# Optimization experiments

Hardware: AMD Instinct MI355X
Metric: run time of the kernel (lower is better)

## Reference

```python
import jax, jax.numpy as jnp
import numpy as np

N, IN_DIM, OUT_DIM = 8192, 512, 512
ALPHA = 0.2  # leaky relu negative slope
NEG_BIG = -9e15

def _xavier(key, shape, gain=1.414):
    fan_in, fan_out = shape[0], shape[1]
    bound = gain * np.sqrt(6.0 / (fan_in + fan_out))
    return jax.random.uniform(key, shape, jnp.float32, -bound, bound)

def setup_inputs() -> dict:
    key = jax.random.key(0)
    k1, k2, k3, k4 = jax.random.split(key, 4)
    h = jax.random.normal(k1, (N, IN_DIM), jnp.float32)
    adj = jax.random.randint(k2, (N, N), 0, 2, jnp.int32)
    W = _xavier(k3, (IN_DIM, OUT_DIM))
    a = _xavier(k4, (2 * OUT_DIM, 1))
    return {"h": h, "adj": adj, "W": W, "a": a}

def reference(h, adj, W, a):
    Wh = h @ W                              # [N, out]
    # e_ij = leakyrelu(a1 . Wh_i + a2 . Wh_j) without the O(N^2*2d) concat
    a1 = a[:OUT_DIM, 0]                     # [out]
    a2 = a[OUT_DIM:, 0]                     # [out]
    f1 = Wh @ a1                            # [N]
    f2 = Wh @ a2                            # [N]
    e = jax.nn.leaky_relu(f1[:, None] + f2[None, :], negative_slope=ALPHA)
    e = jnp.where(adj > 0, e, NEG_BIG)
    attention = jax.nn.softmax(e, axis=1)   # dropout is identity in eval mode
    h_prime = attention @ Wh                # [N, out]
    return jax.nn.elu(h_prime)              # concat=True branch
```

## Files before the change

### kernel.cpp

```cpp
#include <hip/hip_runtime.h>
#include <stdint.h>

#define NN   8192
#define DIN  512
#define DOUT 512
#define ALPHA 0.2f

typedef float          floatx4  __attribute__((ext_vector_type(4)));
typedef float          floatx2  __attribute__((ext_vector_type(2)));
typedef short          shortx8  __attribute__((ext_vector_type(8)));
typedef unsigned short ushortx4 __attribute__((ext_vector_type(4)));
typedef int            intx2    __attribute__((ext_vector_type(2)));

__device__ inline unsigned short f2bf(float x) {
    union { float f; unsigned u; } v; v.f = x;
    return (unsigned short)((v.u + 0x7FFFu + ((v.u >> 16) & 1u)) >> 16);
}
__device__ inline unsigned encf(float x) {
    union { float f; unsigned u; } v; v.f = x;
    return (v.u & 0x80000000u) ? ~v.u : (v.u | 0x80000000u);
}
__device__ inline float decf(unsigned e) {
    union { float f; unsigned u; } v;
    v.u = (e & 0x80000000u) ? (e & 0x7FFFFFFFu) : ~e;
    return v.f;
}
__device__ inline float lrelu(float x) { return fmaxf(x, ALPHA * x); }

__global__ __launch_bounds__(256) void transpose_w(const float* __restrict__ W,
                                                   unsigned short* __restrict__ WT) {
    __shared__ float tile[32][33];
    const int t = threadIdx.x;
    const int x = t & 31, y = t >> 5;
    const int tr = (blockIdx.x >> 4) * 32, tc = (blockIdx.x & 15) * 32;
#pragma unroll
    for (int i = 0; i < 4; i++) {
        int r = y + i * 8;
        tile[r][x] = W[(size_t)(tr + r) * DOUT + tc + x];
    }
    __syncthreads();
#pragma unroll
    for (int i = 0; i < 4; i++) {
        int r = y + i * 8;
        WT[(size_t)(tc + r) * DIN + tr + x] = f2bf(tile[x][r]);
    }
}

__global__ __launch_bounds__(256) void gemm_wh(
    const float* __restrict__ h, const unsigned short* __restrict__ WT,
    const float* __restrict__ a, unsigned short* __restrict__ WhTt,
    float* __restrict__ f1, float* __restrict__ f2, unsigned* __restrict__ Menc)
{
    __shared__ float f1s[4][16], f2s[4][16];
    const int t = threadIdx.x;
    const int w = t >> 6, lane = t & 63, l15 = lane & 15, q = lane >> 4;
    const int r0 = blockIdx.x * 16;
    const int wc0 = w * 128;

    floatx4 acc[8];
    const floatx4 z4 = {0.f, 0.f, 0.f, 0.f};
#pragma unroll
    for (int j = 0; j < 8; j++) acc[j] = z4;

    const float* hp = &h[(size_t)(r0 + l15) * DIN + q * 8];
    const unsigned short* bp = &WT[(size_t)(wc0 + l15) * DIN + q * 8];

    floatx4 hA[2][2];
    shortx8 bB[2][8];
    hA[0][0] = *(const floatx4*)hp;
    hA[0][1] = *(const floatx4*)(hp + 4);
#pragma unroll
    for (int nt = 0; nt < 8; nt++)
        bB[0][nt] = *(const shortx8*)(bp + (size_t)nt * 16 * DIN);

#pragma unroll 2
    for (int it = 0; it < 16; ++it) {
        const int c = it & 1, n = c ^ 1;
        const int kn = ((it + 1) & 15) * 32;
        hA[n][0] = *(const floatx4*)(hp + kn);
        hA[n][1] = *(const floatx4*)(hp + kn + 4);
#pragma unroll
        for (int nt = 0; nt < 8; nt++)
            bB[n][nt] = *(const shortx8*)(bp + (size_t)nt * 16 * DIN + kn);

        shortx8 af;
#pragma unroll
        for (int j = 0; j < 8; j++)
            af[j] = (short)f2bf(hA[c][j >> 2][j & 3]);
#pragma unroll
        for (int nt = 0; nt < 8; nt++)
            acc[nt] = __builtin_amdgcn_mfma_f32_16x16x32_bf16(af, bB[c][nt], acc[nt], 0, 0, 0);
    }

    float a1v[8], a2v[8];
#pragma unroll
    for (int nt = 0; nt < 8; nt++) {
        int col = wc0 + nt * 16 + l15;
        a1v[nt] = a[col];
        a2v[nt] = a[DOUT + col];
    }
    {
        const int kk0 = r0 + q * 4;
        const int tile_k = kk0 >> 5;
        const int qq = (kk0 >> 3) & 3;
        const int j0 = kk0 & 7;
#pragma unroll
        for (int nt = 0; nt < 8; nt++) {
            const int tile_n = w * 8 + nt;
            ushortx4 pk;
#pragma unroll
            for (int reg = 0; reg < 4; reg++) pk[reg] = f2bf(acc[nt][reg]);
            *(ushortx4*)&WhTt[(((size_t)tile_k * 32 + tile_n) << 9) + qq * 128 + l15 * 8 + j0] = pk;
        }
    }
    float s1a[4], s2a[4];
#pragma unroll
    for (int reg = 0; reg < 4; reg++) {
        float s1 = 0.f, s2 = 0.f;
#pragma unroll
        for (int nt = 0; nt < 8; nt++) {
            s1 += acc[nt][reg] * a1v[nt];
            s2 += acc[nt][reg] * a2v[nt];
        }
        s1 += __shfl_xor(s1, 1, 64); s2 += __shfl_xor(s2, 1, 64);
        s1 += __shfl_xor(s1, 2, 64); s2 += __shfl_xor(s2, 2, 64);
        s1 += __shfl_xor(s1, 4, 64); s2 += __shfl_xor(s2, 4, 64);
        s1 += __shfl_xor(s1, 8, 64); s2 += __shfl_xor(s2, 8, 64);
        s1a[reg] = s1; s2a[reg] = s2;
    }
    if (l15 == 0) {
#pragma unroll
        for (int reg = 0; reg < 4; reg++) {
            f1s[w][q * 4 + reg] = s1a[reg];
            f2s[w][q * 4 + reg] = s2a[reg];
        }
    }
    __syncthreads();
    if (t < 16) {
        float v1 = f1s[0][t] + f1s[1][t] + f1s[2][t] + f1s[3][t];
        float v2 = f2s[0][t] + f2s[1][t] + f2s[2][t] + f2s[3][t];
        f1[r0 + t] = v1;
        f2[r0 + t] = v2;
        float mx = v2;
        mx = fmaxf(mx, __shfl_xor(mx, 1, 64));
        mx = fmaxf(mx, __shfl_xor(mx, 2, 64));
        mx = fmaxf(mx, __shfl_xor(mx, 4, 64));
        mx = fmaxf(mx, __shfl_xor(mx, 8, 64));
        if (t == 0) atomicMax(Menc, encf(mx));
    }
}

__global__ __launch_bounds__(1024, 4) void gat_agg(
    const int* __restrict__ adj, const unsigned short* __restrict__ WhTt,
    const float* __restrict__ f1, const float* __restrict__ f2,
    const unsigned* __restrict__ Menc, float* __restrict__ out)
{
    __shared__ __align__(16) unsigned short pbuf[2][2][32 * 40];
    __shared__ float red2[32][260];
    __shared__ float lsp[2][16][32];
    __shared__ float linv[32];

    const int t = threadIdx.x;
    const int w = t >> 6, lane = t & 63, l15 = lane & 15, q = lane >> 4;
    const int ks = w >> 3, cw = w & 7;
    const int u = cw * 64 + lane;
    const int prow = u >> 4, pkc = u & 15;
    const int r0 = blockIdx.x * 32;

    const float M = decf(*Menc);
    const float f1v = f1[r0 + prow];
    const float mi = lrelu(f1v + M);

    floatx4 acc[2][4];
    const floatx4 z4 = {0.f, 0.f, 0.f, 0.f};
#pragma unroll
    for (int i = 0; i < 2; i++)
#pragma unroll
        for (int j = 0; j < 4; j++) acc[i][j] = z4;
    float ls = 0.f;

    const unsigned short* bpp = WhTt + (((size_t)(ks * 128) * 32 + cw * 4) << 9) + lane * 8;
    const int* arp = adj + (size_t)(r0 + prow) * NN + ks * 4096 + pkc * 2;
    const float* fpp = f2 + ks * 4096 + pkc * 2;

    intx2    adjr[2];
    floatx2  ffr[2];
    shortx8  breg[2][4];

    adjr[0] = __builtin_nontemporal_load((const intx2*)arp);
    adjr[1] = __builtin_nontemporal_load((const intx2*)(arp + 32));
    ffr[0] = *(const floatx2*)fpp;
    ffr[1] = *(const floatx2*)(fpp + 32);
    {
        float p0 = __expf(lrelu(f1v + ffr[0][0]) - mi);
        float p1 = __expf(lrelu(f1v + ffr[0][1]) - mi);
        p0 = (adjr[0][0] > 0) ? p0 : 0.f;
        p1 = (adjr[0][1] > 0) ? p1 : 0.f;
        ls += p0 + p1;
        unsigned d = __builtin_amdgcn_perm(__float_as_uint(p1), __float_as_uint(p0), 0x07060302u);
        *(unsigned*)&pbuf[ks][0][prow * 40 + pkc * 2] = d;
    }
#pragma unroll
    for (int nt = 0; nt < 4; nt++)
        breg[0][nt] = *(const shortx8*)(bpp + nt * 512);
    __syncthreads();

#pragma unroll 2
    for (int it = 0; it < 128; ++it) {
        const int c = it & 1, n = c ^ 1;
        const int nx = (it + 1) & 127;
        const int nx2 = (it + 2) & 127;

#pragma unroll
        for (int nt = 0; nt < 4; nt++)
            breg[n][nt] = *(const shortx8*)(bpp + (size_t)nx * 16384 + nt * 512);
        const intx2   ad_n = adjr[n];
        const floatx2 ff_n = ffr[n];
        adjr[c] = __builtin_nontemporal_load((const intx2*)(arp + nx2 * 32));
        ffr[c] = *(const floatx2*)(fpp + nx2 * 32);

        if (it < 127) {
            float p0 = __expf(lrelu(f1v + ff_n[0]) - mi);
            float p1 = __expf(lrelu(f1v + ff_n[1]) - mi);
            p0 = (ad_n[0] > 0) ? p0 : 0.f;
            p1 = (ad_n[1] > 0) ? p1 : 0.f;
            ls += p0 + p1;
            unsigned d = __builtin_amdgcn_perm(__float_as_uint(p1), __float_as_uint(p0), 0x07060302u);
            *(unsigned*)&pbuf[ks][n][prow * 40 + pkc * 2] = d;
        }

        const shortx8 af0 = *(const shortx8*)&pbuf[ks][c][l15 * 40 + q * 8];
        const shortx8 af1 = *(const shortx8*)&pbuf[ks][c][(16 + l15) * 40 + q * 8];
#pragma unroll
        for (int nt = 0; nt < 4; nt++) {
            acc[0][nt] = __builtin_amdgcn_mfma_f32_16x16x32_bf16(af0, breg[c][nt], acc[0][nt], 0, 0, 0);
            acc[1][nt] = __builtin_amdgcn_mfma_f32_16x16x32_bf16(af1, breg[c][nt], acc[1][nt], 0, 0, 0);
        }
        __syncthreads();
    }

    lsp[ks][pkc][prow] = ls;
    __syncthreads();
    if (t < 32) {
        float s = 0.f;
#pragma unroll
        for (int g = 0; g < 2; g++)
#pragma unroll
            for (int kc = 0; kc < 16; kc++) s += lsp[g][kc][t];
        linv[t] = 1.f / s;
    }
    __syncthreads();

#pragma unroll 1
    for (int half = 0; half < 2; ++half) {
        const int inHalf = (cw >> 2) == half;
        const int colb = (cw & 3) * 64;
        if (ks == 1 && inHalf) {
#pragma unroll
            for (int mt = 0; mt < 2; mt++)
#pragma unroll
                for (int nt = 0; nt < 4; nt++) {
                    const int col = colb + nt * 16 + l15;
#pragma unroll
                    for (int reg = 0; reg < 4; reg++)
                        red2[mt * 16 + q * 4 + reg][col] = acc[mt][nt][reg];
                }
        }
        __syncthreads();
        if (ks == 0 && inHalf) {
#pragma unroll
            for (int mt = 0; mt < 2; mt++)
#pragma unroll
                for (int nt = 0; nt < 4; nt++) {
                    const int col = colb + nt * 16 + l15;
#pragma unroll
                    for (int reg = 0; reg < 4; reg++) {
                        const int row = mt * 16 + q * 4 + reg;
                        float x = (acc[mt][nt][reg] + red2[row][col]) * linv[row];
                        x = (x > 0.f) ? x : (__expf(x) - 1.f);
                        out[(size_t)(r0 + row) * DOUT + half * 256 + col] = x;
                    }
                }
        }
        __syncthreads();
    }
}

extern "C" void kernel_launch(void* const* d_in, const int* in_sizes, int n_in,
                              void* d_out, int out_size, void* d_ws, size_t ws_size,
                              hipStream_t stream) {
    const float* h   = (const float*)d_in[0];
    const int*   adj = (const int*)d_in[1];
    const float* W   = (const float*)d_in[2];
    const float* a   = (const float*)d_in[3];
    float* out = (float*)d_out;

    char* ws = (char*)d_ws;
    unsigned short* WT    = (unsigned short*)ws;
    unsigned short* WhTt  = (unsigned short*)(ws + 524288);
    float*          f1    = (float*)(ws + 8912896);
    float*          f2    = (float*)(ws + 8945664);
    unsigned*       Menc  = (unsigned*)(ws + 8978432);

    hipMemsetAsync(Menc, 0, 4, stream);
    transpose_w<<<256, 256, 0, stream>>>(W, WT);
    gemm_wh<<<512, 256, 0, stream>>>(h, WT, a, WhTt, f1, f2, Menc);
    gat_agg<<<256, 1024, 0, stream>>>(adj, WhTt, f1, f2, Menc, out);
}
```

Measured before the change: 509.7 us.

## Retile GAT aggregation to 64 rows × 256 cols with XCD-aware block mapping

Each aggregation block now covers 64 output rows and half of the 512 feature columns, where it used to cover 32 rows and all columns. This halves the per-block streaming of the transposed Wh operand and doubles the reuse of each B fragment across four MFMA row tiles. Blocks are remapped so the two column halves of one row group land on the same XCD, hoping adjacency reads hit in the shared L2. In exchange, each adjacency row and its exp/leaky-relu probabilities are read and computed twice, once per column half, and the epilogue is simplified to a single reduction pass.

```diff
diff --git a/kernel.cpp b/kernel.cpp
--- a/kernel.cpp
+++ b/kernel.cpp
@@ -11,6 +11,8 @@
 typedef short          shortx8  __attribute__((ext_vector_type(8)));
 typedef unsigned short ushortx4 __attribute__((ext_vector_type(4)));
 typedef int            intx2    __attribute__((ext_vector_type(2)));
+typedef int            intx4    __attribute__((ext_vector_type(4)));
+typedef unsigned       uintx2   __attribute__((ext_vector_type(2)));
 
 __device__ inline unsigned short f2bf(float x) {
     union { float f; unsigned u; } v; v.f = x;
@@ -155,54 +157,65 @@
     const float* __restrict__ f1, const float* __restrict__ f2,
     const unsigned* __restrict__ Menc, float* __restrict__ out)
 {
-    __shared__ __align__(16) unsigned short pbuf[2][2][32 * 40];
-    __shared__ float red2[32][260];
-    __shared__ float lsp[2][16][32];
-    __shared__ float linv[32];
+    __shared__ __align__(16) unsigned short pbuf[2][2][64 * 40];
+    __shared__ float red2[64][260];
+    __shared__ float lsp[2][8][64];
+    __shared__ float linv[64];
 
     const int t = threadIdx.x;
     const int w = t >> 6, lane = t & 63, l15 = lane & 15, q = lane >> 4;
     const int ks = w >> 3, cw = w & 7;
-    const int u = cw * 64 + lane;
-    const int prow = u >> 4, pkc = u & 15;
-    const int r0 = blockIdx.x * 32;
+    const int u = (w & 7) * 64 + lane;
+    const int prow = u >> 3, pk = u & 7;
+
+    const int xcd = blockIdx.x & 7, sidx = blockIdx.x >> 3;
+    const int chalf = sidx & 1;
+    const int rgid = xcd * 16 + (sidx >> 1);
+    const int r0 = rgid * 64;
+    const int cb = chalf * 256;
 
     const float M = decf(*Menc);
     const float f1v = f1[r0 + prow];
     const float mi = lrelu(f1v + M);
 
-    floatx4 acc[2][4];
+    floatx4 acc[4][2];
     const floatx4 z4 = {0.f, 0.f, 0.f, 0.f};
 #pragma unroll
-    for (int i = 0; i < 2; i++)
-#pragma unroll
-        for (int j = 0; j < 4; j++) acc[i][j] = z4;
+    for (int i = 0; i < 4; i++)
+#pragma unroll
+        for (int j = 0; j < 2; j++) acc[i][j] = z4;
     float ls = 0.f;
 
-    const unsigned short* bpp = WhTt + (((size_t)(ks * 128) * 32 + cw * 4) << 9) + lane * 8;
-    const int* arp = adj + (size_t)(r0 + prow) * NN + ks * 4096 + pkc * 2;
-    const float* fpp = f2 + ks * 4096 + pkc * 2;
-
-    intx2    adjr[2];
-    floatx2  ffr[2];
-    shortx8  breg[2][4];
-
-    adjr[0] = __builtin_nontemporal_load((const intx2*)arp);
-    adjr[1] = __builtin_nontemporal_load((const intx2*)(arp + 32));
-    ffr[0] = *(const floatx2*)fpp;
-    ffr[1] = *(const floatx2*)(fpp + 32);
+    const unsigned short* bpp = WhTt
+        + (((size_t)(ks * 128) * 32 + chalf * 16 + cw * 2) << 9) + lane * 8;
+    const int* arp = adj + (size_t)(r0 + prow) * NN + ks * 4096 + pk * 4;
+    const float* fpp = f2 + ks * 4096 + pk * 4;
+
+    intx4   adjr[2];
+    floatx4 ffr[2];
+    shortx8 breg[2][2];
+
+    adjr[0] = __builtin_nontemporal_load((const intx4*)arp);
+    adjr[1] = __builtin_nontemporal_load((const intx4*)(arp + 32));
+    ffr[0] = *(const floatx4*)fpp;
+    ffr[1] = *(const floatx4*)(fpp + 32);
     {
         float p0 = __expf(lrelu(f1v + ffr[0][0]) - mi);
         float p1 = __expf(lrelu(f1v + ffr[0][1]) - mi);
+        float p2 = __expf(lrelu(f1v + ffr[0][2]) - mi);
+        float p3 = __expf(lrelu(f1v + ffr[0][3]) - mi);
         p0 = (adjr[0][0] > 0) ? p0 : 0.f;
         p1 = (adjr[0][1] > 0) ? p1 : 0.f;
-        ls += p0 + p1;
-        unsigned d = __builtin_amdgcn_perm(__float_as_uint(p1), __float_as_uint(p0), 0x07060302u);
-        *(unsigned*)&pbuf[ks][0][prow * 40 + pkc * 2] = d;
-    }
-#pragma unroll
-    for (int nt = 0; nt < 4; nt++)
-        breg[0][nt] = *(const shortx8*)(bpp + nt * 512);
+        p2 = (adjr[0][2] > 0) ? p2 : 0.f;
+        p3 = (adjr[0][3] > 0) ? p3 : 0.f;
+        ls += (p0 + p1) + (p2 + p3);
+        uintx2 dd;
+        dd[0] = __builtin_amdgcn_perm(__float_as_uint(p1), __float_as_uint(p0), 0x07060302u);
+        dd[1] = __builtin_amdgcn_perm(__float_as_uint(p3), __float_as_uint(p2), 0x07060302u);
+        *(uintx2*)&pbuf[ks][0][prow * 40 + pk * 4] = dd;
+    }
+    breg[0][0] = *(const shortx8*)bpp;
+    breg[0][1] = *(const shortx8*)(bpp + 512);
     __syncthreads();
 
 #pragma unroll 2
@@ -211,78 +224,79 @@
         const int nx = (it + 1) & 127;
         const int nx2 = (it + 2) & 127;
 
-#pragma unroll
-        for (int nt = 0; nt < 4; nt++)
-            breg[n][nt] = *(const shortx8*)(bpp + (size_t)nx * 16384 + nt * 512);
-        const intx2   ad_n = adjr[n];
-        const floatx2 ff_n = ffr[n];
-        adjr[c] = __builtin_nontemporal_load((const intx2*)(arp + nx2 * 32));
-        ffr[c] = *(const floatx2*)(fpp + nx2 * 32);
+        breg[n][0] = *(const shortx8*)(bpp + (size_t)nx * 16384);
+        breg[n][1] = *(const shortx8*)(bpp + (size_t)nx * 16384 + 512);
+        const intx4   ad_n = adjr[n];
+        const floatx4 ff_n = ffr[n];
+        adjr[c] = __builtin_nontemporal_load((const intx4*)(arp + nx2 * 32));
+        ffr[c] = *(const floatx4*)(fpp + nx2 * 32);
 
         if (it < 127) {
             float p0 = __expf(lrelu(f1v + ff_n[0]) - mi);
             float p1 = __expf(lrelu(f1v + ff_n[1]) - mi);
+            float p2 = __expf(lrelu(f1v + ff_n[2]) - mi);
+            float p3 = __expf(lrelu(f1v + ff_n[3]) - mi);
             p0 = (ad_n[0] > 0) ? p0 : 0.f;
             p1 = (ad_n[1] > 0) ? p1 : 0.f;
-            ls += p0 + p1;
-            unsigned d = __builtin_amdgcn_perm(__float_as_uint(p1), __float_as_uint(p0), 0x07060302u);
-            *(unsigned*)&pbuf[ks][n][prow * 40 + pkc * 2] = d;
-        }
-
-        const shortx8 af0 = *(const shortx8*)&pbuf[ks][c][l15 * 40 + q * 8];
+            p2 = (ad_n[2] > 0) ? p2 : 0.f;
+            p3 = (ad_n[3] > 0) ? p3 : 0.f;
+            ls += (p0 + p1) + (p2 + p3);
+            uintx2 dd;
+            dd[0] = __builtin_amdgcn_perm(__float_as_uint(p1), __float_as_uint(p0), 0x07060302u);
+            dd[1] = __builtin_amdgcn_perm(__float_as_uint(p3), __float_as_uint(p2), 0x07060302u);
+            *(uintx2*)&pbuf[ks][n][prow * 40 + pk * 4] = dd;
+        }
+
+        const shortx8 af0 = *(const shortx8*)&pbuf[ks][c][(l15) * 40 + q * 8];
         const shortx8 af1 = *(const shortx8*)&pbuf[ks][c][(16 + l15) * 40 + q * 8];
-#pragma unroll
-        for (int nt = 0; nt < 4; nt++) {
+        const shortx8 af2 = *(const shortx8*)&pbuf[ks][c][(32 + l15) * 40 + q * 8];
+        const shortx8 af3 = *(const shortx8*)&pbuf[ks][c][(48 + l15) * 40 + q * 8];
+#pragma unroll
+        for (int nt = 0; nt < 2; nt++) {
             acc[0][nt] = __builtin_amdgcn_mfma_f32_16x16x32_bf16(af0, breg[c][nt], acc[0][nt], 0, 0, 0);
             acc[1][nt] = __builtin_amdgcn_mfma_f32_16x16x32_bf16(af1, breg[c][nt], acc[1][nt], 0, 0, 0);
+            acc[2][nt] = __builtin_amdgcn_mfma_f32_16x16x32_bf16(af2, breg[c][nt], acc[2][nt], 0, 0, 0);
+            acc[3][nt] = __builtin_amdgcn_mfma_f32_16x16x32_bf16(af3, breg[c][nt], acc[3][nt], 0, 0, 0);
         }
         __syncthreads();
     }
 
-    lsp[ks][pkc][prow] = ls;
-    __syncthreads();
-    if (t < 32) {
-        float s = 0.f;
+    lsp[ks][pk][prow] = ls;
+    __syncthreads();
+    if (t < 64) {
+        float sden = 0.f;
 #pragma unroll
         for (int g = 0; g < 2; g++)
 #pragma unroll
-            for (int kc = 0; kc < 16; kc++) s += lsp[g][kc][t];
-        linv[t] = 1.f / s;
-    }
-    __syncthreads();
-
-#pragma unroll 1
-    for (int half = 0; half < 2; ++half) {
-        const int inHalf = (cw >> 2) == half;
-        const int colb = (cw & 3) * 64;
-        if (ks == 1 && inHalf) {
-#pragma unroll
-            for (int mt = 0; mt < 2; mt++)
-#pragma unroll
-                for (int nt = 0; nt < 4; nt++) {
-                    const int col = colb + nt * 16 + l15;
-#pragma unroll
-                    for (int reg = 0; reg < 4; reg++)
-                        red2[mt * 16 + q * 4 + reg][col] = acc[mt][nt][reg];
+            for (int kc = 0; kc < 8; kc++) sden += lsp[g][kc][t];
+        linv[t] = 1.f / sden;
+    }
+    if (ks == 1) {
+#pragma unroll
+        for (int mt = 0; mt < 4; mt++)
+#pragma unroll
+            for (int nt = 0; nt < 2; nt++) {
+                const int col = cw * 32 + nt * 16 + l15;
+#pragma unroll
+                for (int reg = 0; reg < 4; reg++)
+                    red2[mt * 16 + q * 4 + reg][col] = acc[mt][nt][reg];
+            }
+    }
+    __syncthreads();
+    if (ks == 0) {
+#pragma unroll
+        for (int mt = 0; mt < 4; mt++)
+#pragma unroll
+            for (int nt = 0; nt < 2; nt++) {
+                const int col = cw * 32 + nt * 16 + l15;
+#pragma unroll
+                for (int reg = 0; reg < 4; reg++) {
+                    const int row = mt * 16 + q * 4 + reg;
+                    float v = (acc[mt][nt][reg] + red2[row][col]) * linv[row];
+                    v = (v > 0.f) ? v : (__expf(v) - 1.f);
+                    out[(size_t)(r0 + row) * DOUT + cb + col] = v;
                 }
-        }
-        __syncthreads();
-        if (ks == 0 && inHalf) {
-#pragma unroll
-            for (int mt = 0; mt < 2; mt++)
-#pragma unroll
-                for (int nt = 0; nt < 4; nt++) {
-                    const int col = colb + nt * 16 + l15;
-#pragma unroll
-                    for (int reg = 0; reg < 4; reg++) {
-                        const int row = mt * 16 + q * 4 + reg;
-                        float x = (acc[mt][nt][reg] + red2[row][col]) * linv[row];
-                        x = (x > 0.f) ? x : (__expf(x) - 1.f);
-                        out[(size_t)(r0 + row) * DOUT + half * 256 + col] = x;
-                    }
-                }
-        }
-        __syncthreads();
+            }
     }
 }
 
```

Measured after the change: 466.4 us. 1.09x faster.
